# Kernel optimization log

Measured on AMD Instinct MI355X. Metric: run time of the kernel, lower is better.

The kernel has to match this reference:

```python
import jax, jax.numpy as jnp
from jax import lax
import numpy as np

B, T = 32, 15
THR1, THR2 = 15.0, 10.0  # conv1_t, conv2_t


def _conv(x, w):
    # x: (B,T,C,H,W) cumulative potentials/spikes; conv applied per timestep
    b, t, c, h, wd = x.shape
    y = lax.conv_general_dilated(x.reshape(b * t, c, h, wd), w, (1, 1), 'VALID',
                                 dimension_numbers=('NCHW', 'OIHW', 'NCHW'))
    return y.reshape(b, t, *y.shape[1:])


def _pool(x, k, s):
    b, t, c, h, wd = x.shape
    y = lax.reduce_window(x.reshape(b * t, c, h, wd), -jnp.inf, lax.max,
                          (1, 1, k, k), (1, 1, s, s), 'VALID')
    return y.reshape(b, t, *y.shape[1:])


def _pad(x, p):
    return jnp.pad(x, ((0, 0), (0, 0), (0, 0), (p, p), (p, p)))


def _fire(pot, thr):
    # sf.fire: F.threshold_(pot, thr, 0); spk = sign
    th = jnp.where(pot > thr, pot, 0.0)
    return jnp.sign(th), th


def _winner_class(pot, spk):
    # sf.get_k_winners(pot, kwta=1, r=0, spk): earliest spike, tie-break by potential
    b, t = spk.shape[:2]
    cnt = spk.sum(axis=1)                                   # (B,F,H,W) spike counts
    first = jnp.clip((t - cnt).astype(jnp.int32), 0, t - 1)  # earliest spike time
    vals = jnp.take_along_axis(pot, first[:, None], axis=1)[:, 0]  # pot at spike time
    trunc = spk * vals[:, None]                              # (B,T,F,H,W)
    v = trunc.reshape(b, -1).max(axis=1) * t                 # dominance offset per sample
    total = (trunc + spk * v[:, None, None, None, None]).sum(axis=1)  # (B,F,H,W)
    flat = total.reshape(b, -1)
    idx = jnp.argmax(flat, axis=1)
    mx = jnp.max(flat, axis=1)
    hw = pot.shape[-1] * pot.shape[-2]
    feat = idx // hw
    # decision_map: 10 classes x 20 features each -> class = feat // 20; -1 if no spike
    return jnp.where(mx != 0, feat // 20, -1).astype(jnp.int32)


def setup_inputs() -> dict:
    key = jax.random.key(0)
    k1, k2, k3, k4 = jax.random.split(key, 4)
    # cumulative binary spike wave: neuron fires at t_fire and stays 1 afterwards
    t_fire = jax.random.randint(k1, (B, 18, 32, 32), 0, T + 1)
    inp = (jnp.arange(T)[None, :, None, None, None] >= t_fire[:, None]).astype(jnp.float32)
    w1 = 0.8 + 0.05 * jax.random.normal(k2, (90, 18, 7, 7), dtype=jnp.float32)
    w2 = 0.8 + 0.05 * jax.random.normal(k3, (250, 90, 5, 5), dtype=jnp.float32)
    w3 = 0.8 + 0.05 * jax.random.normal(k4, (200, 250, 5, 5), dtype=jnp.float32)
    return {'input': inp, 'w1': w1, 'w2': w2, 'w3': w3, 'max_layer': 3}


def reference(input, w1, w2, w3, max_layer):
    # eval-mode forward of CIFAR10Net
    x = _pad(input, 2)                       # (B,T,18,36,36)
    spk1, pot1 = _fire(_conv(x, w1), THR1)   # (B,T,90,30,30)
    if max_layer == 1:
        return spk1, pot1
    spk2, pot2 = _fire(_conv(_pad(_pool(spk1, 2, 2), 1), w2), THR2)  # (B,T,250,13,13)
    if max_layer == 2:
        return spk2, pot2
    pot3 = _conv(_pad(_pool(spk2, 3, 3), 2), w3)   # (B,T,200,4,4)
    t = pot3.shape[1]
    mask = (jnp.arange(t) == t - 1).astype(pot3.dtype)[None, :, None, None, None]
    spk3 = jnp.sign(pot3 * mask)             # fire with threshold=None: only last step
    cls = _winner_class(pot3, spk3)          # (B,) predicted class or -1
    return cls, pot3
```

## Files before the change

kernel.cpp:

```cpp
#include <hip/hip_runtime.h>

#define NB 32
#define NT 15


__device__ __forceinline__ float gather8(const int* lst, int i, const char* wb) {
    int4 p0 = *(const int4*)(lst + i);
    int4 p1 = *(const int4*)(lst + i + 4);
    int o0 = __builtin_amdgcn_readfirstlane(p0.x);
    int o1 = __builtin_amdgcn_readfirstlane(p0.y);
    int o2 = __builtin_amdgcn_readfirstlane(p0.z);
    int o3 = __builtin_amdgcn_readfirstlane(p0.w);
    int o4 = __builtin_amdgcn_readfirstlane(p1.x);
    int o5 = __builtin_amdgcn_readfirstlane(p1.y);
    int o6 = __builtin_amdgcn_readfirstlane(p1.z);
    int o7 = __builtin_amdgcn_readfirstlane(p1.w);
    float a0 = *(const float*)(wb + o0);
    float a1 = *(const float*)(wb + o1);
    float a2 = *(const float*)(wb + o2);
    float a3 = *(const float*)(wb + o3);
    float a4 = *(const float*)(wb + o4);
    float a5 = *(const float*)(wb + o5);
    float a6 = *(const float*)(wb + o6);
    float a7 = *(const float*)(wb + o7);
    return ((a0 + a1) + (a2 + a3)) + ((a4 + a5) + (a6 + a7));
}

__device__ __forceinline__ void tr_tile(const float* __restrict__ src, float* __restrict__ dst,
                                        int F, int K, int KK, int CIN, int nkt, int t, int tid) {
    __shared__ float lds[32][33];
    int kt = t % nkt, ft = t / nkt;
    int k0 = kt * 32, f0 = ft * 32;
    int tx = tid & 31, ty = tid >> 5;
#pragma unroll
    for (int i = 0; i < 4; i++) {
        int fl = ty + 8 * i;
        int f = f0 + fl, k = k0 + tx;
        lds[fl][tx] = (f < F && k < K) ? src[(size_t)f * K + k] : 0.f;
    }
    __syncthreads();
#pragma unroll
    for (int i = 0; i < 4; i++) {
        int row = ty + 8 * i;
        int k = k0 + row, f = f0 + tx;
        if (k < K && f < F) {
            int j = (k % KK) * CIN + k / KK;
            dst[(size_t)j * F + f] = lds[tx][row];
        }
    }
}

__global__ __launch_bounds__(256) void k_pre(const float* __restrict__ inp,
                                             const float* __restrict__ w1,
                                             const float* __restrict__ w2,
                                             const float* __restrict__ w3,
                                             float* __restrict__ wT1, float* __restrict__ wT2,
                                             float* __restrict__ wT3,
                                             unsigned char* __restrict__ zmap,
                                             float* __restrict__ PosS2, float* __restrict__ PosS3,
                                             float* __restrict__ Pmin1,
                                             unsigned char* __restrict__ ft1,
                                             unsigned char* __restrict__ zmaps) {
    int blk = blockIdx.x, tid = threadIdx.x;
    if (blk < 2024) {
        const float* src; float* dst;
        int F, K, KK, CIN, nkt, t;
        if (blk < 84)       { src = w1; dst = wT1; F = 90;  K = 882;  KK = 49; CIN = 18;  nkt = 28;  t = blk; }
        else if (blk < 652) { src = w2; dst = wT2; F = 250; K = 2250; KK = 25; CIN = 90;  nkt = 71;  t = blk - 84; }
        else                { src = w3; dst = wT3; F = 200; K = 6250; KK = 25; CIN = 250; nkt = 196; t = blk - 652; }
        tr_tile(src, dst, F, K, KK, CIN, nkt, t, tid);
    } else if (blk == 2024) {
        if (tid < 90)  wT1[882 * 90 + tid] = 0.f;
        if (tid < 250) wT2[(size_t)2250 * 250 + tid] = 0.f;
        if (tid < 200) wT3[(size_t)6250 * 200 + tid] = 0.f;
    } else if (blk < 2187) {
        int idx = (blk - 2025) * 256 + tid;
        int xx = idx % 36, rest = idx / 36;
        int yy = rest % 36; int b = rest / 36;
        int z = 0;
        int x = xx - 2, y = yy - 2;
        if (x >= 0 && x < 32 && y >= 0 && y < 32) {
            const float* p = inp + (size_t)b * NT * 18 * 1024 + y * 32 + x;
#pragma unroll
            for (int c = 0; c < 18; c++) z += (p[(size_t)c * 1024] != 0.f);
        }
        zmap[idx] = (unsigned char)z;
    } else if (blk < 2212) {
        int idx = (blk - 2187) * 256 + tid;
        if (idx < 6250) {
            int f = idx / 25, pos = idx - f * 25;
            float acc = 0.f;
            for (int c = 0; c < 90; c++) acc += w2[(size_t)(f * 90 + c) * 25 + pos];
            PosS2[pos * 256 + f] = acc;
        }
    } else if (blk < 2232) {
        int idx = (blk - 2212) * 256 + tid;
        if (idx < 5000) {
            int f = idx / 25, pos = idx - f * 25;
            float acc = 0.f;
            for (int c = 0; c < 250; c++) acc += w3[(size_t)(f * 250 + c) * 25 + pos];
            PosS3[pos * 200 + f] = acc;
        }
    } else if (blk < 2272) {
        int bb = blk - 2232;
        __shared__ float wm[4];
        float m = 1e30f;
#pragma unroll
        for (int k = 0; k < 8; k++) {
            int i = bb * 2048 + k * 256 + tid;
            if (i < 90 * 882) m = fminf(m, w1[i]);
        }
        for (int o = 32; o > 0; o >>= 1) m = fminf(m, __shfl_down(m, o));
        if ((tid & 63) == 0) wm[tid >> 6] = m;
        __syncthreads();
        if (tid == 0) Pmin1[bb] = fminf(fminf(wm[0], wm[1]), fminf(wm[2], wm[3]));
    } else if (blk < 2905) {
        int i = (blk - 2272) * 256 + tid;
        if (i < 162000) ((uint4*)ft1)[i] = uint4{0, 0, 0, 0};
    } else {
        int i = (blk - 2905) * 256 + tid;
        if (i < 2150) ((uint4*)zmaps)[i] = uint4{0, 0, 0, 0};
    }
}

__global__ __launch_bounds__(256) void k_screen1(const unsigned char* __restrict__ zmap,
                                                 const float* __restrict__ Pmin1,
                                                 const float* __restrict__ PosS2,
                                                 const float* __restrict__ PosS3,
                                                 float* __restrict__ W2e, float* __restrict__ W3s,
                                                 int* __restrict__ cnt, int* __restrict__ list1) {
    int blk = blockIdx.x, tid = threadIdx.x;
    if (blk < 113) {
        int idx = blk * 256 + tid;
        if (idx < 28800) {
            int b = idx / 900, p = idx - b * 900;
            int oy = p / 30, ox = p - oy * 30;
            float m1 = 1e30f;
            for (int i = 0; i < 40; i++) m1 = fminf(m1, Pmin1[i]);
            int c0 = 0;
            const unsigned char* zb = zmap + (b * 36 + oy) * 36 + ox;
#pragma unroll
            for (int dy = 0; dy < 7; dy++)
#pragma unroll
                for (int dx = 0; dx < 7; dx++) c0 += zb[dy * 36 + dx];
            if (!((float)c0 * m1 > 15.0f)) {
                int pos = atomicAdd(cnt + 0, 1);
                list1[pos] = idx;
            }
        }
    } else if (blk < 282) {
        int p = blk - 113;
        int oy = p / 13, ox = p - oy * 13;
        int f = tid < 250 ? tid : 249;
        float W = 0.f;
#pragma unroll
        for (int pos = 0; pos < 25; pos++) {
            int r = pos / 5, x = pos - r * 5;
            int gy = oy + r, gx = ox + x;
            if (!(gy == 0 || gy == 16 || gx == 0 || gx == 16)) W += PosS2[pos * 256 + f];
        }
        if (tid < 250) W2e[p * 256 + tid] = W;
    } else {
        int i = (blk - 282) * 256 + tid;
        if (i < 3200) {
            int px = i / 200, f = i - px * 200;
            int oy = px >> 2, ox = px & 3;
            int r0 = max(0, 2 - oy), r1 = min(4, 5 - oy);
            int x0 = max(0, 2 - ox), x1 = min(4, 5 - ox);
            float s = 0.f;
            for (int r = r0; r <= r1; r++)
                for (int x = x0; x <= x1; x++) s += PosS3[(r * 5 + x) * 200 + f];
            W3s[px * 200 + f] = s;
        }
    }
}

__global__ __launch_bounds__(256) void k_hard1_fill(const float* __restrict__ inp,
                                                    const float* __restrict__ wT1,
                                                    const float* __restrict__ W2e,
                                                    const float* __restrict__ W3s,
                                                    const int* __restrict__ cnt,
                                                    const int* __restrict__ list1,
                                                    unsigned char* __restrict__ ft1,
                                                    unsigned char* __restrict__ nzc1,
                                                    unsigned char* __restrict__ ft2,
                                                    unsigned char* __restrict__ nz2any,
                                                    float* __restrict__ out) {
    __shared__ __align__(16) int slist[896];
    __shared__ int scnt, spcnt;
    int blk = blockIdx.x, tid = threadIdx.x;
    if (blk < 900) {
        int n = cnt[0];
        for (int it = blk; it < n; it += 900) {
            __syncthreads();
            int idx = list1[it];
            int b = idx / 900, p = idx - b * 900;
            int oy = p / 30, ox = p - oy * 30;
            unsigned char myft[4];
#pragma unroll
            for (int k = 0; k < 4; k++) {
                int j = tid + k * 256;
                unsigned char v = 255;
                if (j < 882) {
                    int dy = j / 126, rem = j - dy * 126;
                    int dx = rem / 18, c = rem - dx * 18;
                    int y = oy + dy - 2, x = ox + dx - 2;
                    v = 15;
                    if ((unsigned)y < 32u && (unsigned)x < 32u)
                        v = (inp[(size_t)b * 276480 + (size_t)c * 1024 + y * 32 + x] != 0.f) ? 0 : 200;
                }
                myft[k] = v;
            }
            int f = tid < 90 ? tid : 89;
            const char* wb = (const char*)(wT1 + f);
            const int zoff = 882 * 90 * 4;
            float acc = 0.f; int ftv = 15;
            for (int s = 0; s < 15; s++) {
                if (s == 1) {
#pragma unroll
                    for (int k = 0; k < 4; k++) {
                        if (myft[k] == 200) {
                            int j = tid + k * 256;
                            int dy = j / 126, rem = j - dy * 126;
                            int dx = rem / 18, c = rem - dx * 18;
                            int y = oy + dy - 2, x = ox + dx - 2;
                            const float* q = inp + (size_t)b * 276480 + (size_t)c * 1024 + y * 32 + x;
                            int cf = 0;
#pragma unroll
                            for (int t = 1; t < NT; t++) cf += (q[(size_t)t * 18432] != 0.f);
                            myft[k] = (unsigned char)(15 - cf);
                        }
                    }
                }
                if (tid == 0) scnt = 0;
                __syncthreads();
#pragma unroll
                for (int k = 0; k < 4; k++) {
                    if ((int)myft[k] == s) { int pp = atomicAdd(&scnt, 1); slist[pp] = (tid + k * 256) * 360; }
                }
                __syncthreads();
                if (tid == 0) {
                    int c0 = scnt, cp = (c0 + 7) & ~7;
                    for (int i = c0; i < cp; i++) slist[i] = zoff;
                    spcnt = cp;
                }
                __syncthreads();
                int e = spcnt;
                for (int i = 0; i < e; i += 8) acc += gather8(slist, i, wb);
                if (ftv == 15 && acc > 15.0f) ftv = s;
                if (__syncthreads_and(ftv != 15)) break;
            }
            if (tid < 90) {
                ft1[(size_t)idx * 90 + tid] = (unsigned char)ftv;
                if (ftv != 0) nzc1[idx] = 1;
            }
        }
    } else if (blk < 1231) {
        int i = (blk - 900) * 256 + tid;
        if (i < 84500) {
            union { unsigned char c[16]; uint4 v; } u;
            int g = i * 16;
#pragma unroll
            for (int k = 0; k < 16; k++) {
                int gg = g + k;
                int f = gg % 250;
                int p = (gg / 250) % 169;
                u.c[k] = (W2e[p * 256 + f] > 10.0f) ? 0 : 15;
            }
            *(uint4*)(ft2 + (size_t)g) = u.v;
        }
    } else if (blk == 1231) {
        if (tid < 169) {
            unsigned char any = 0;
            for (int f = 0; f < 250; f++) any |= (W2e[tid * 256 + f] <= 10.0f) ? 1 : 0;
            nz2any[tid] = any;
        }
    } else {
        int i = (blk - 1232) * 256 + tid;
        int g = i * 4;
        int px0 = g & 15;
        int f = (g >> 4) % 200;
        float4 v;
        v.x = W3s[(px0 + 0) * 200 + f];
        v.y = W3s[(px0 + 1) * 200 + f];
        v.z = W3s[(px0 + 2) * 200 + f];
        v.w = W3s[(px0 + 3) * 200 + f];
        *(float4*)(out + 32 + (size_t)g) = v;
    }
}

__global__ __launch_bounds__(256) void k_screen2(const unsigned char* __restrict__ nzc1,
                                                 const unsigned char* __restrict__ nz2any,
                                                 unsigned char* __restrict__ nzc2,
                                                 int* __restrict__ cnt, int* __restrict__ list2) {
    int idx = blockIdx.x * 256 + threadIdx.x;
    if (idx >= 5408) return;
    int b = idx / 169, p = idx - b * 169;
    int oy = p / 13, ox = p - oy * 13;
    int gy0 = max(1, oy), gy1 = min(15, oy + 4);
    int gx0 = max(1, ox), gx1 = min(15, ox + 4);
    int y0 = 2 * (gy0 - 1), y1 = 2 * (gy1 - 1) + 1;
    int x0 = 2 * (gx0 - 1), x1 = 2 * (gx1 - 1) + 1;
    int s = 0;
    const unsigned char* nb = nzc1 + b * 900;
    for (int y = y0; y <= y1; y++)
        for (int x = x0; x <= x1; x++) s += nb[y * 30 + x];
    nzc2[idx] = nz2any[p];
    if (s) { int pos = atomicAdd(cnt + 1, 1); list2[pos] = idx; }
}

__global__ __launch_bounds__(256) void k_hard2(const unsigned char* __restrict__ ft1,
                                               const float* __restrict__ wT2,
                                               const float* __restrict__ W2e,
                                               const int* __restrict__ cnt,
                                               const int* __restrict__ list2,
                                               unsigned char* __restrict__ ft2,
                                               unsigned char* __restrict__ nzc2) {
    constexpr int PADCAP = 2250 + 15 * 8;
    __shared__ __align__(16) int perm[PADCAP];
    __shared__ int start[16], cur[16];
    __shared__ int cntCs, anynz;
    int tid = threadIdx.x;
    int n = cnt[1];
    for (int it = blockIdx.x; it < n; it += 512) {
        __syncthreads();
        int idx = list2[it];
        int b = idx / 169, p = idx - b * 169;
        int oy = p / 13, ox = p - oy * 13;
        const unsigned char* fb = ft1 + (size_t)b * 81000;
        if (tid == 0) { cntCs = 0; anynz = 0; }
        if (tid < 16) cur[tid] = 0;
        unsigned char myft[9];
        int nc = 0;
#pragma unroll
        for (int k = 0; k < 9; k++) {
            int j = tid + k * 256;
            myft[k] = 0;
            if (j < 2250) {
                int r = j / 450, rem = j - r * 450;
                int x = rem / 90, c = rem - x * 90;
                int gy = oy + r, gx = ox + x;
                if (gy >= 1 && gy <= 15 && gx >= 1 && gx <= 15) {
                    const unsigned char* q = fb + ((size_t)((gy - 1) * 2) * 30 + (gx - 1) * 2) * 90 + c;
                    int m = q[0];
                    m = min(m, (int)q[90]);
                    m = min(m, (int)q[2700]);
                    m = min(m, (int)q[2790]);
                    myft[k] = (unsigned char)m;
                }
            }
            nc += (myft[k] >= 1);
        }
        for (int o = 32; o > 0; o >>= 1) nc += __shfl_down(nc, o);
        __syncthreads();
        if ((tid & 63) == 0) atomicAdd(&cntCs, nc);
        __syncthreads();
        int f = tid < 250 ? tid : 249;
        float W = W2e[p * 256 + f];
        int ftv;
        if (cntCs == 0) {
            ftv = (W > 10.0f) ? 0 : 15;
        } else {
#pragma unroll
            for (int k = 0; k < 9; k++) { int v = myft[k]; if (v >= 1) atomicAdd(&cur[v - 1], 1); }
            __syncthreads();
            if (tid == 0) {
                int s = 0;
#pragma unroll
                for (int j = 0; j < 15; j++) { int c = cur[j]; start[j] = s; s += (c + 7) & ~7; }
                start[15] = s;
            }
            __syncthreads();
            int nnzp = start[15];
            if (tid < 15) cur[tid] = start[tid];
            const int zoff = 2250 * 250 * 4;
            for (int i = tid; i < nnzp; i += 256) perm[i] = zoff;
            __syncthreads();
#pragma unroll
            for (int k = 0; k < 9; k++) {
                int v = myft[k];
                if (v >= 1) { int pp = atomicAdd(&cur[v - 1], 1); perm[pp] = (tid + k * 256) * 1000; }
            }
            __syncthreads();
            const char* wb = (const char*)(wT2 + f);
            float R = 0.f; int ft = 15;
            for (int j = 14; j >= 0; j--) {
                int sjb = start[j], e = start[j + 1];
                for (int i = sjb; i < e; i += 8) R += gather8(perm, i, wb);
                float pot = W - R;
                if (pot > 10.0f) ft = j;
                if (sjb == 0) { if (pot > 10.0f) ft = 0; break; }
                if (__all(pot <= 10.0f)) break;
            }
            ftv = ft;
        }
        if (tid < 250) {
            ft2[(size_t)idx * 250 + tid] = (unsigned char)ftv;
            if (ftv != 0) anynz = 1;
        }
        __syncthreads();
        if (tid == 0) nzc2[idx] = (unsigned char)(anynz ? 1 : 0);
    }
}

__global__ __launch_bounds__(256) void k_screen3(const unsigned char* __restrict__ nzc2,
                                                 int* __restrict__ cnt, int* __restrict__ list3) {
    int idx = blockIdx.x * 256 + threadIdx.x;
    if (idx >= 512) return;
    int b = idx >> 4, p = idx & 15;
    int oy = p >> 2, ox = p & 3;
    int r0 = max(0, 2 - oy), r1 = min(4, 5 - oy);
    int x0 = max(0, 2 - ox), x1 = min(4, 5 - ox);
    int py0 = oy + r0 - 2, py1 = oy + r1 - 2;
    int qx0 = ox + x0 - 2, qx1 = ox + x1 - 2;
    int s = 0;
    const unsigned char* nb = nzc2 + b * 169;
    for (int y = 3 * py0; y <= 3 * py1 + 2; y++)
        for (int x = 3 * qx0; x <= 3 * qx1 + 2; x++) s += nb[y * 13 + x];
    if (s) { int pos = atomicAdd(cnt + 2, 1); list3[pos] = idx; }
}

__global__ __launch_bounds__(256) void k_hard3(const unsigned char* __restrict__ ft2,
                                               const float* __restrict__ wT3,
                                               const float* __restrict__ W3s,
                                               const int* __restrict__ cnt,
                                               const int* __restrict__ list3,
                                               float* __restrict__ out) {
    constexpr int PADCAP = 4000 + 15 * 8;
    __shared__ __align__(16) int perm[PADCAP];
    __shared__ int start[16], cur[16];
    __shared__ int fbs[16], rowb[16];
    int tid = threadIdx.x;
    int n = cnt[2];
    for (int it = blockIdx.x; it < n; it += 256) {
        __syncthreads();
        int idx = list3[it];
        int b = idx >> 4, p = idx & 15;
        int oy = p >> 2, ox = p & 3;
        int r0 = max(0, 2 - oy), r1 = min(4, 5 - oy);
        int x0 = max(0, 2 - ox), x1 = min(4, 5 - ox);
        int VR = r1 - r0 + 1, VC = x1 - x0 + 1;
        int NP = VR * VC, NV = NP * 250;
        const unsigned char* fb = ft2 + (size_t)b * 42250;
        if (tid < NP) {
            int rv = tid / VC, xv = tid - rv * VC;
            int py = oy + r0 + rv - 2, pxx = ox + x0 + xv - 2;
            fbs[tid]  = (py * 3 * 13 + pxx * 3) * 250;
            rowb[tid] = ((r0 + rv) * 5 + (x0 + xv)) * 250;
        }
        if (tid < 16) cur[tid] = 0;
        __syncthreads();
        unsigned char myft[16];
#pragma unroll
        for (int k = 0; k < 16; k++) {
            int i = tid + k * 256;
            myft[k] = 0;
            if (i < NV) {
                int posv = i / 250, c = i - posv * 250;
                const unsigned char* q = fb + fbs[posv] + c;
                int m = q[0];
#pragma unroll
                for (int dy = 0; dy < 3; dy++)
#pragma unroll
                    for (int dx = 0; dx < 3; dx++)
                        if (dy | dx) m = min(m, (int)q[(dy * 13 + dx) * 250]);
                myft[k] = (unsigned char)m;
            }
        }
#pragma unroll
        for (int k = 0; k < 16; k++) { int v = myft[k]; if (v >= 1) atomicAdd(&cur[v - 1], 1); }
        __syncthreads();
        if (tid == 0) {
            int s = 0;
#pragma unroll
            for (int j = 0; j < 15; j++) { int c = cur[j]; start[j] = s; s += (c + 7) & ~7; }
            start[15] = s;
        }
        __syncthreads();
        int nnzp = start[15];
        if (tid < 15) cur[tid] = start[tid];
        const int zoff = 6250 * 200 * 4;
        for (int i = tid; i < nnzp; i += 256) perm[i] = zoff;
        __syncthreads();
#pragma unroll
        for (int k = 0; k < 16; k++) {
            int v = myft[k];
            if (v >= 1) {
                int i = tid + k * 256;
                int posv = i / 250, c = i - posv * 250;
                int pp = atomicAdd(&cur[v - 1], 1);
                perm[pp] = (rowb[posv] + c) * 800;
            }
        }
        __syncthreads();

        int f = tid < 200 ? tid : 199;
        const char* wb = (const char*)(wT3 + f);
        float W = W3s[p * 200 + f];
        float* o = out + 32 + ((size_t)b * NT) * 3200 + f * 16 + p;
        float R = 0.f;
        for (int j = 14; j >= 0; j--) {
            int sjb = start[j], e = start[j + 1];
            for (int i = sjb; i < e; i += 8) R += gather8(perm, i, wb);
            float pot = W - R;
            if (tid < 200) o[(size_t)j * 3200] = pot;
            if (sjb == 0) {
                for (int jj = j - 1; jj >= 0; jj--)
                    if (tid < 200) o[(size_t)jj * 3200] = pot;
                break;
            }
        }
    }
}

__global__ __launch_bounds__(256) void k_winner(const float* __restrict__ outp,
                                                float* __restrict__ outc) {
    int b = blockIdx.x, tid = threadIdx.x;
    const float* p14 = outp + 32 + ((size_t)b * NT + 14) * 3200;
    __shared__ float sv[256];
    __shared__ int   si[256];
    float m = 0.f;
    for (int j = tid; j < 3200; j += 256) {
        float v = p14[j];
        if (v > 0.f && v > m) m = v;
    }
    sv[tid] = m;
    __syncthreads();
    for (int s = 128; s > 0; s >>= 1) {
        if (tid < s) sv[tid] = fmaxf(sv[tid], sv[tid + s]);
        __syncthreads();
    }
    float vofs = 15.f * sv[0];
    __syncthreads();
    float bestv = 0.f; int besti = 0x3fffffff;
    for (int j = tid; j < 3200; j += 256) {
        float v = p14[j];
        float tot = (v > 0.f) ? v + vofs : 0.f;
        if (tot > bestv) { bestv = tot; besti = j; }
    }
    sv[tid] = bestv; si[tid] = besti;
    __syncthreads();
    for (int s = 128; s > 0; s >>= 1) {
        if (tid < s) {
            if (sv[tid + s] > sv[tid] || (sv[tid + s] == sv[tid] && si[tid + s] < si[tid])) {
                sv[tid] = sv[tid + s]; si[tid] = si[tid + s];
            }
        }
        __syncthreads();
    }
    if (tid == 0) {
        float mx = sv[0];
        int cls = (mx != 0.f) ? ((si[0] / 16) / 20) : -1;
        outc[b] = (float)cls;
    }
}

extern "C" void kernel_launch(void* const* d_in, const int* in_sizes, int n_in,
                              void* d_out, int out_size, void* d_ws, size_t ws_size,
                              hipStream_t stream) {
    const float* inp = (const float*)d_in[0];
    const float* w1  = (const float*)d_in[1];
    const float* w2  = (const float*)d_in[2];
    const float* w3  = (const float*)d_in[3];
    float* out = (float*)d_out;

    unsigned char* ws   = (unsigned char*)d_ws;
    unsigned char* ft1  = ws + 0;
    unsigned char* ft2  = ws + 2592000;
    float* wT1   = (float*)(ws + 3944000);
    float* wT2   = (float*)(ws + 4261888);
    float* wT3   = (float*)(ws + 6512896);
    float* PosS2 = (float*)(ws + 11513728);
    float* PosS3 = (float*)(ws + 11539328);
    float* W2e   = (float*)(ws + 11559328);
    float* W3s   = (float*)(ws + 11732384);
    float* Pmin1 = (float*)(ws + 11745184);
    unsigned char* zmap   = ws + 11745440;
    unsigned char* nzc1   = ws + 11786912;
    unsigned char* nzc2   = ws + 11815712;
    unsigned char* nz2any = ws + 11821120;
    int* cnt    = (int*)(ws + 11821296);
    int* list1  = (int*)(ws + 11821312);
    int* list2  = (int*)(ws + 11936512);
    int* list3  = (int*)(ws + 11958144);

    hipLaunchKernelGGL(k_pre, dim3(2914), dim3(256), 0, stream,
                       inp, w1, w2, w3, wT1, wT2, wT3, zmap, PosS2, PosS3, Pmin1, ft1, nzc1);
    hipLaunchKernelGGL(k_screen1, dim3(295), dim3(256), 0, stream,
                       zmap, Pmin1, PosS2, PosS3, W2e, W3s, cnt, list1);
    hipLaunchKernelGGL(k_hard1_fill, dim3(2732), dim3(256), 0, stream,
                       inp, wT1, W2e, W3s, cnt, list1, ft1, nzc1, ft2, nz2any, out);
    hipLaunchKernelGGL(k_screen2, dim3(22), dim3(256), 0, stream, nzc1, nz2any, nzc2, cnt, list2);
    hipLaunchKernelGGL(k_hard2, dim3(512), dim3(256), 0, stream, ft1, wT2, W2e, cnt, list2, ft2, nzc2);
    hipLaunchKernelGGL(k_screen3, dim3(2), dim3(256), 0, stream, nzc2, cnt, list3);
    hipLaunchKernelGGL(k_hard3, dim3(256), dim3(256), 0, stream, ft2, wT3, W3s, cnt, list3, out);
    hipLaunchKernelGGL(k_winner, dim3(NB), dim3(256), 0, stream, out, out);
}
```

Baseline: 155.8 us.

## Fuse all stages into one persistent kernel with grid-wide atomic barriers

Merges the eight separate kernel launches into a single persistent kernel of 256 blocks. Each former launch becomes a grid-stride loop over virtual blocks, and stages are separated by a global atomic-counter barrier reset by a memset. This is meant to remove per-launch overhead and the drain/fill gaps between dependent stages. In exchange, the stages with large grids (2914 and 2732 blocks) now run with only 256 resident blocks, the barriers spin-wait, and correctness depends on all blocks being co-resident.

```diff
diff --git a/kernel.cpp b/kernel.cpp
--- a/kernel.cpp
+++ b/kernel.cpp
@@ -2,7 +2,20 @@
 
 #define NB 32
 #define NT 15
-
+#define NBLK 256
+
+
+__device__ __forceinline__ void gbar(int* bar, int id) {
+    __syncthreads();
+    if (threadIdx.x == 0) {
+        __threadfence();
+        __hip_atomic_fetch_add(&bar[id], 1, __ATOMIC_ACQ_REL, __HIP_MEMORY_SCOPE_AGENT);
+        while (__hip_atomic_load(&bar[id], __ATOMIC_ACQUIRE, __HIP_MEMORY_SCOPE_AGENT) < NBLK)
+            __builtin_amdgcn_s_sleep(1);
+        __threadfence();
+    }
+    __syncthreads();
+}
 
 __device__ __forceinline__ float gather8(const int* lst, int i, const char* wb) {
     int4 p0 = *(const int4*)(lst + i);
@@ -48,150 +61,147 @@
             dst[(size_t)j * F + f] = lds[tx][row];
         }
     }
+    __syncthreads();
 }
 
-__global__ __launch_bounds__(256) void k_pre(const float* __restrict__ inp,
+__global__ __launch_bounds__(256) void k_all(const float* __restrict__ inp,
                                              const float* __restrict__ w1,
                                              const float* __restrict__ w2,
                                              const float* __restrict__ w3,
                                              float* __restrict__ wT1, float* __restrict__ wT2,
                                              float* __restrict__ wT3,
+                                             float* __restrict__ PosS2, float* __restrict__ PosS3,
+                                             float* __restrict__ W2e, float* __restrict__ W3s,
+                                             float* __restrict__ Pmin1,
                                              unsigned char* __restrict__ zmap,
-                                             float* __restrict__ PosS2, float* __restrict__ PosS3,
-                                             float* __restrict__ Pmin1,
                                              unsigned char* __restrict__ ft1,
-                                             unsigned char* __restrict__ zmaps) {
+                                             unsigned char* __restrict__ ft2,
+                                             unsigned char* __restrict__ nzc1,
+                                             unsigned char* __restrict__ nzc2,
+                                             unsigned char* __restrict__ nz2any,
+                                             int* __restrict__ cnt,
+                                             int* __restrict__ list1, int* __restrict__ list2,
+                                             int* __restrict__ list3,
+                                             int* __restrict__ bar,
+                                             float* __restrict__ out) {
     int blk = blockIdx.x, tid = threadIdx.x;
-    if (blk < 2024) {
-        const float* src; float* dst;
-        int F, K, KK, CIN, nkt, t;
-        if (blk < 84)       { src = w1; dst = wT1; F = 90;  K = 882;  KK = 49; CIN = 18;  nkt = 28;  t = blk; }
-        else if (blk < 652) { src = w2; dst = wT2; F = 250; K = 2250; KK = 25; CIN = 90;  nkt = 71;  t = blk - 84; }
-        else                { src = w3; dst = wT3; F = 200; K = 6250; KK = 25; CIN = 250; nkt = 196; t = blk - 652; }
-        tr_tile(src, dst, F, K, KK, CIN, nkt, t, tid);
-    } else if (blk == 2024) {
-        if (tid < 90)  wT1[882 * 90 + tid] = 0.f;
-        if (tid < 250) wT2[(size_t)2250 * 250 + tid] = 0.f;
-        if (tid < 200) wT3[(size_t)6250 * 200 + tid] = 0.f;
-    } else if (blk < 2187) {
-        int idx = (blk - 2025) * 256 + tid;
-        int xx = idx % 36, rest = idx / 36;
-        int yy = rest % 36; int b = rest / 36;
-        int z = 0;
-        int x = xx - 2, y = yy - 2;
-        if (x >= 0 && x < 32 && y >= 0 && y < 32) {
-            const float* p = inp + (size_t)b * NT * 18 * 1024 + y * 32 + x;
-#pragma unroll
-            for (int c = 0; c < 18; c++) z += (p[(size_t)c * 1024] != 0.f);
-        }
-        zmap[idx] = (unsigned char)z;
-    } else if (blk < 2212) {
-        int idx = (blk - 2187) * 256 + tid;
-        if (idx < 6250) {
-            int f = idx / 25, pos = idx - f * 25;
-            float acc = 0.f;
-            for (int c = 0; c < 90; c++) acc += w2[(size_t)(f * 90 + c) * 25 + pos];
-            PosS2[pos * 256 + f] = acc;
-        }
-    } else if (blk < 2232) {
-        int idx = (blk - 2212) * 256 + tid;
-        if (idx < 5000) {
-            int f = idx / 25, pos = idx - f * 25;
-            float acc = 0.f;
-            for (int c = 0; c < 250; c++) acc += w3[(size_t)(f * 250 + c) * 25 + pos];
-            PosS3[pos * 200 + f] = acc;
-        }
-    } else if (blk < 2272) {
-        int bb = blk - 2232;
-        __shared__ float wm[4];
-        float m = 1e30f;
-#pragma unroll
-        for (int k = 0; k < 8; k++) {
-            int i = bb * 2048 + k * 256 + tid;
-            if (i < 90 * 882) m = fminf(m, w1[i]);
-        }
-        for (int o = 32; o > 0; o >>= 1) m = fminf(m, __shfl_down(m, o));
-        if ((tid & 63) == 0) wm[tid >> 6] = m;
-        __syncthreads();
-        if (tid == 0) Pmin1[bb] = fminf(fminf(wm[0], wm[1]), fminf(wm[2], wm[3]));
-    } else if (blk < 2905) {
-        int i = (blk - 2272) * 256 + tid;
-        if (i < 162000) ((uint4*)ft1)[i] = uint4{0, 0, 0, 0};
-    } else {
-        int i = (blk - 2905) * 256 + tid;
-        if (i < 2150) ((uint4*)zmaps)[i] = uint4{0, 0, 0, 0};
-    }
-}
-
-__global__ __launch_bounds__(256) void k_screen1(const unsigned char* __restrict__ zmap,
-                                                 const float* __restrict__ Pmin1,
-                                                 const float* __restrict__ PosS2,
-                                                 const float* __restrict__ PosS3,
-                                                 float* __restrict__ W2e, float* __restrict__ W3s,
-                                                 int* __restrict__ cnt, int* __restrict__ list1) {
-    int blk = blockIdx.x, tid = threadIdx.x;
-    if (blk < 113) {
-        int idx = blk * 256 + tid;
-        if (idx < 28800) {
-            int b = idx / 900, p = idx - b * 900;
-            int oy = p / 30, ox = p - oy * 30;
-            float m1 = 1e30f;
-            for (int i = 0; i < 40; i++) m1 = fminf(m1, Pmin1[i]);
-            int c0 = 0;
-            const unsigned char* zb = zmap + (b * 36 + oy) * 36 + ox;
-#pragma unroll
-            for (int dy = 0; dy < 7; dy++)
-#pragma unroll
-                for (int dx = 0; dx < 7; dx++) c0 += zb[dy * 36 + dx];
-            if (!((float)c0 * m1 > 15.0f)) {
-                int pos = atomicAdd(cnt + 0, 1);
-                list1[pos] = idx;
-            }
-        }
-    } else if (blk < 282) {
-        int p = blk - 113;
-        int oy = p / 13, ox = p - oy * 13;
-        int f = tid < 250 ? tid : 249;
-        float W = 0.f;
-#pragma unroll
-        for (int pos = 0; pos < 25; pos++) {
-            int r = pos / 5, x = pos - r * 5;
-            int gy = oy + r, gx = ox + x;
-            if (!(gy == 0 || gy == 16 || gx == 0 || gx == 16)) W += PosS2[pos * 256 + f];
-        }
-        if (tid < 250) W2e[p * 256 + tid] = W;
-    } else {
-        int i = (blk - 282) * 256 + tid;
-        if (i < 3200) {
-            int px = i / 200, f = i - px * 200;
-            int oy = px >> 2, ox = px & 3;
-            int r0 = max(0, 2 - oy), r1 = min(4, 5 - oy);
-            int x0 = max(0, 2 - ox), x1 = min(4, 5 - ox);
-            float s = 0.f;
-            for (int r = r0; r <= r1; r++)
-                for (int x = x0; x <= x1; x++) s += PosS3[(r * 5 + x) * 200 + f];
-            W3s[px * 200 + f] = s;
-        }
-    }
-}
-
-__global__ __launch_bounds__(256) void k_hard1_fill(const float* __restrict__ inp,
-                                                    const float* __restrict__ wT1,
-                                                    const float* __restrict__ W2e,
-                                                    const float* __restrict__ W3s,
-                                                    const int* __restrict__ cnt,
-                                                    const int* __restrict__ list1,
-                                                    unsigned char* __restrict__ ft1,
-                                                    unsigned char* __restrict__ nzc1,
-                                                    unsigned char* __restrict__ ft2,
-                                                    unsigned char* __restrict__ nz2any,
-                                                    float* __restrict__ out) {
-    __shared__ __align__(16) int slist[896];
-    __shared__ int scnt, spcnt;
-    int blk = blockIdx.x, tid = threadIdx.x;
-    if (blk < 900) {
-        int n = cnt[0];
-        for (int it = blk; it < n; it += 900) {
+
+    for (int vb = blk; vb < 2914; vb += NBLK) {
+        if (vb < 2024) {
+            const float* src; float* dst;
+            int F, K, KK, CIN, nkt, t;
+            if (vb < 84)       { src = w1; dst = wT1; F = 90;  K = 882;  KK = 49; CIN = 18;  nkt = 28;  t = vb; }
+            else if (vb < 652) { src = w2; dst = wT2; F = 250; K = 2250; KK = 25; CIN = 90;  nkt = 71;  t = vb - 84; }
+            else               { src = w3; dst = wT3; F = 200; K = 6250; KK = 25; CIN = 250; nkt = 196; t = vb - 652; }
+            tr_tile(src, dst, F, K, KK, CIN, nkt, t, tid);
+        } else if (vb == 2024) {
+            if (tid < 90)  wT1[882 * 90 + tid] = 0.f;
+            if (tid < 250) wT2[(size_t)2250 * 250 + tid] = 0.f;
+            if (tid < 200) wT3[(size_t)6250 * 200 + tid] = 0.f;
+        } else if (vb < 2187) {
+            int idx = (vb - 2025) * 256 + tid;
+            int xx = idx % 36, rest = idx / 36;
+            int yy = rest % 36; int b = rest / 36;
+            int z = 0;
+            int x = xx - 2, y = yy - 2;
+            if (x >= 0 && x < 32 && y >= 0 && y < 32) {
+                const float* p = inp + (size_t)b * NT * 18 * 1024 + y * 32 + x;
+#pragma unroll
+                for (int c = 0; c < 18; c++) z += (p[(size_t)c * 1024] != 0.f);
+            }
+            zmap[idx] = (unsigned char)z;
+        } else if (vb < 2212) {
+            int idx = (vb - 2187) * 256 + tid;
+            if (idx < 6250) {
+                int f = idx / 25, pos = idx - f * 25;
+                float acc = 0.f;
+                for (int c = 0; c < 90; c++) acc += w2[(size_t)(f * 90 + c) * 25 + pos];
+                PosS2[pos * 256 + f] = acc;
+            }
+        } else if (vb < 2232) {
+            int idx = (vb - 2212) * 256 + tid;
+            if (idx < 5000) {
+                int f = idx / 25, pos = idx - f * 25;
+                float acc = 0.f;
+                for (int c = 0; c < 250; c++) acc += w3[(size_t)(f * 250 + c) * 25 + pos];
+                PosS3[pos * 200 + f] = acc;
+            }
+        } else if (vb < 2272) {
+            int bb = vb - 2232;
+            __shared__ float wm[4];
+            float m = 1e30f;
+#pragma unroll
+            for (int k = 0; k < 8; k++) {
+                int i = bb * 2048 + k * 256 + tid;
+                if (i < 90 * 882) m = fminf(m, w1[i]);
+            }
+            for (int o = 32; o > 0; o >>= 1) m = fminf(m, __shfl_down(m, o));
+            if ((tid & 63) == 0) wm[tid >> 6] = m;
+            __syncthreads();
+            if (tid == 0) Pmin1[bb] = fminf(fminf(wm[0], wm[1]), fminf(wm[2], wm[3]));
+            __syncthreads();
+        } else if (vb < 2905) {
+            int i = (vb - 2272) * 256 + tid;
+            if (i < 162000) ((uint4*)ft1)[i] = uint4{0, 0, 0, 0};
+        } else {
+            int i = (vb - 2905) * 256 + tid;
+            if (i < 2150) ((uint4*)nzc1)[i] = uint4{0, 0, 0, 0};
+        }
+    }
+    gbar(bar, 0);
+
+    for (int vb = blk; vb < 295; vb += NBLK) {
+        if (vb < 113) {
+            int idx = vb * 256 + tid;
+            if (idx < 28800) {
+                int b = idx / 900, p = idx - b * 900;
+                int oy = p / 30, ox = p - oy * 30;
+                float m1 = 1e30f;
+                for (int i = 0; i < 40; i++) m1 = fminf(m1, Pmin1[i]);
+                int c0 = 0;
+                const unsigned char* zb = zmap + (b * 36 + oy) * 36 + ox;
+#pragma unroll
+                for (int dy = 0; dy < 7; dy++)
+#pragma unroll
+                    for (int dx = 0; dx < 7; dx++) c0 += zb[dy * 36 + dx];
+                if (!((float)c0 * m1 > 15.0f)) {
+                    int pos = atomicAdd(cnt + 0, 1);
+                    list1[pos] = idx;
+                }
+            }
+        } else if (vb < 282) {
+            int p = vb - 113;
+            int oy = p / 13, ox = p - oy * 13;
+            int f = tid < 250 ? tid : 249;
+            float W = 0.f;
+#pragma unroll
+            for (int pos = 0; pos < 25; pos++) {
+                int r = pos / 5, x = pos - r * 5;
+                int gy = oy + r, gx = ox + x;
+                if (!(gy == 0 || gy == 16 || gx == 0 || gx == 16)) W += PosS2[pos * 256 + f];
+            }
+            if (tid < 250) W2e[p * 256 + tid] = W;
+        } else {
+            int i = (vb - 282) * 256 + tid;
+            if (i < 3200) {
+                int px = i / 200, f = i - px * 200;
+                int oy = px >> 2, ox = px & 3;
+                int r0 = max(0, 2 - oy), r1 = min(4, 5 - oy);
+                int x0 = max(0, 2 - ox), x1 = min(4, 5 - ox);
+                float s = 0.f;
+                for (int r = r0; r <= r1; r++)
+                    for (int x = x0; x <= x1; x++) s += PosS3[(r * 5 + x) * 200 + f];
+                W3s[px * 200 + f] = s;
+            }
+        }
+    }
+    gbar(bar, 1);
+
+    {
+        __shared__ __align__(16) int slist[896];
+        __shared__ int scnt, spcnt;
+        int n1 = __hip_atomic_load(&cnt[0], __ATOMIC_RELAXED, __HIP_MEMORY_SCOPE_AGENT);
+        for (int it = blk; it < n1; it += NBLK) {
             __syncthreads();
             int idx = list1[it];
             int b = idx / 900, p = idx - b * 900;
@@ -254,115 +264,214 @@
                 ft1[(size_t)idx * 90 + tid] = (unsigned char)ftv;
                 if (ftv != 0) nzc1[idx] = 1;
             }
-        }
-    } else if (blk < 1231) {
-        int i = (blk - 900) * 256 + tid;
-        if (i < 84500) {
-            union { unsigned char c[16]; uint4 v; } u;
-            int g = i * 16;
+            __syncthreads();
+        }
+        for (int vb = blk; vb < 1832; vb += NBLK) {
+            if (vb < 331) {
+                int i = vb * 256 + tid;
+                if (i < 84500) {
+                    union { unsigned char c[16]; uint4 v; } u;
+                    int g = i * 16;
+#pragma unroll
+                    for (int k = 0; k < 16; k++) {
+                        int gg = g + k;
+                        int f = gg % 250;
+                        int p = (gg / 250) % 169;
+                        u.c[k] = (W2e[p * 256 + f] > 10.0f) ? 0 : 15;
+                    }
+                    *(uint4*)(ft2 + (size_t)g) = u.v;
+                }
+            } else if (vb == 331) {
+                if (tid < 169) {
+                    unsigned char any = 0;
+                    for (int f = 0; f < 250; f++) any |= (W2e[tid * 256 + f] <= 10.0f) ? 1 : 0;
+                    nz2any[tid] = any;
+                }
+            } else {
+                int i = (vb - 332) * 256 + tid;
+                int g = i * 4;
+                int px0 = g & 15;
+                int f = (g >> 4) % 200;
+                float4 v;
+                v.x = W3s[(px0 + 0) * 200 + f];
+                v.y = W3s[(px0 + 1) * 200 + f];
+                v.z = W3s[(px0 + 2) * 200 + f];
+                v.w = W3s[(px0 + 3) * 200 + f];
+                *(float4*)(out + 32 + (size_t)g) = v;
+            }
+        }
+    }
+    gbar(bar, 2);
+
+    {
+        int idx = blk * 256 + tid;
+        if (idx < 5408) {
+            int b = idx / 169, p = idx - b * 169;
+            int oy = p / 13, ox = p - oy * 13;
+            int gy0 = max(1, oy), gy1 = min(15, oy + 4);
+            int gx0 = max(1, ox), gx1 = min(15, ox + 4);
+            int y0 = 2 * (gy0 - 1), y1 = 2 * (gy1 - 1) + 1;
+            int x0 = 2 * (gx0 - 1), x1 = 2 * (gx1 - 1) + 1;
+            int s = 0;
+            const unsigned char* nb = nzc1 + b * 900;
+            for (int y = y0; y <= y1; y++)
+                for (int x = x0; x <= x1; x++) s += nb[y * 30 + x];
+            nzc2[idx] = nz2any[p];
+            if (s) { int pos = atomicAdd(cnt + 1, 1); list2[pos] = idx; }
+        }
+    }
+    gbar(bar, 3);
+
+    {
+        constexpr int PADCAP = 2250 + 15 * 8;
+        __shared__ __align__(16) int perm[PADCAP];
+        __shared__ int start[16], cur[16];
+        __shared__ int cntCs, anynz;
+        int n2 = __hip_atomic_load(&cnt[1], __ATOMIC_RELAXED, __HIP_MEMORY_SCOPE_AGENT);
+        for (int it = blk; it < n2; it += NBLK) {
+            __syncthreads();
+            int idx = list2[it];
+            int b = idx / 169, p = idx - b * 169;
+            int oy = p / 13, ox = p - oy * 13;
+            const unsigned char* fb = ft1 + (size_t)b * 81000;
+            if (tid == 0) { cntCs = 0; anynz = 0; }
+            if (tid < 16) cur[tid] = 0;
+            unsigned char myft[9];
+            int nc = 0;
+#pragma unroll
+            for (int k = 0; k < 9; k++) {
+                int j = tid + k * 256;
+                myft[k] = 0;
+                if (j < 2250) {
+                    int r = j / 450, rem = j - r * 450;
+                    int x = rem / 90, c = rem - x * 90;
+                    int gy = oy + r, gx = ox + x;
+                    if (gy >= 1 && gy <= 15 && gx >= 1 && gx <= 15) {
+                        const unsigned char* q = fb + ((size_t)((gy - 1) * 2) * 30 + (gx - 1) * 2) * 90 + c;
+                        int m = q[0];
+                        m = min(m, (int)q[90]);
+                        m = min(m, (int)q[2700]);
+                        m = min(m, (int)q[2790]);
+                        myft[k] = (unsigned char)m;
+                    }
+                }
+                nc += (myft[k] >= 1);
+            }
+            for (int o = 32; o > 0; o >>= 1) nc += __shfl_down(nc, o);
+            __syncthreads();
+            if ((tid & 63) == 0) atomicAdd(&cntCs, nc);
+            __syncthreads();
+            int f = tid < 250 ? tid : 249;
+            float W = W2e[p * 256 + f];
+            int ftv;
+            if (cntCs == 0) {
+                ftv = (W > 10.0f) ? 0 : 15;
+            } else {
+#pragma unroll
+                for (int k = 0; k < 9; k++) { int v = myft[k]; if (v >= 1) atomicAdd(&cur[v - 1], 1); }
+                __syncthreads();
+                if (tid == 0) {
+                    int s = 0;
+#pragma unroll
+                    for (int j = 0; j < 15; j++) { int c = cur[j]; start[j] = s; s += (c + 7) & ~7; }
+                    start[15] = s;
+                }
+                __syncthreads();
+                int nnzp = start[15];
+                if (tid < 15) cur[tid] = start[tid];
+                const int zoff = 2250 * 250 * 4;
+                for (int i = tid; i < nnzp; i += 256) perm[i] = zoff;
+                __syncthreads();
+#pragma unroll
+                for (int k = 0; k < 9; k++) {
+                    int v = myft[k];
+                    if (v >= 1) { int pp = atomicAdd(&cur[v - 1], 1); perm[pp] = (tid + k * 256) * 1000; }
+                }
+                __syncthreads();
+                const char* wb = (const char*)(wT2 + f);
+                float R = 0.f; int ft = 15;
+                for (int j = 14; j >= 0; j--) {
+                    int sjb = start[j], e = start[j + 1];
+                    for (int i = sjb; i < e; i += 8) R += gather8(perm, i, wb);
+                    float pot = W - R;
+                    if (pot > 10.0f) ft = j;
+                    if (sjb == 0) { if (pot > 10.0f) ft = 0; break; }
+                    if (__all(pot <= 10.0f)) break;
+                }
+                ftv = ft;
+            }
+            if (tid < 250) {
+                ft2[(size_t)idx * 250 + tid] = (unsigned char)ftv;
+                if (ftv != 0) anynz = 1;
+            }
+            __syncthreads();
+            if (tid == 0) nzc2[idx] = (unsigned char)(anynz ? 1 : 0);
+            __syncthreads();
+        }
+    }
+    gbar(bar, 4);
+
+    {
+        int idx = blk * 256 + tid;
+        if (idx < 512) {
+            int b = idx >> 4, p = idx & 15;
+            int oy = p >> 2, ox = p & 3;
+            int r0 = max(0, 2 - oy), r1 = min(4, 5 - oy);
+            int x0 = max(0, 2 - ox), x1 = min(4, 5 - ox);
+            int py0 = oy + r0 - 2, py1 = oy + r1 - 2;
+            int qx0 = ox + x0 - 2, qx1 = ox + x1 - 2;
+            int s = 0;
+            const unsigned char* nb = nzc2 + b * 169;
+            for (int y = 3 * py0; y <= 3 * py1 + 2; y++)
+                for (int x = 3 * qx0; x <= 3 * qx1 + 2; x++) s += nb[y * 13 + x];
+            if (s) { int pos = atomicAdd(cnt + 2, 1); list3[pos] = idx; }
+        }
+    }
+    gbar(bar, 5);
+
+    {
+        constexpr int PADCAP = 4000 + 15 * 8;
+        __shared__ __align__(16) int perm[PADCAP];
+        __shared__ int start[16], cur[16];
+        __shared__ int fbs[16], rowb[16];
+        int n3 = __hip_atomic_load(&cnt[2], __ATOMIC_RELAXED, __HIP_MEMORY_SCOPE_AGENT);
+        for (int it = blk; it < n3; it += NBLK) {
+            __syncthreads();
+            int idx = list3[it];
+            int b = idx >> 4, p = idx & 15;
+            int oy = p >> 2, ox = p & 3;
+            int r0 = max(0, 2 - oy), r1 = min(4, 5 - oy);
+            int x0 = max(0, 2 - ox), x1 = min(4, 5 - ox);
+            int VR = r1 - r0 + 1, VC = x1 - x0 + 1;
+            int NP = VR * VC, NV = NP * 250;
+            const unsigned char* fb = ft2 + (size_t)b * 42250;
+            if (tid < NP) {
+                int rv = tid / VC, xv = tid - rv * VC;
+                int py = oy + r0 + rv - 2, pxx = ox + x0 + xv - 2;
+                fbs[tid]  = (py * 3 * 13 + pxx * 3) * 250;
+                rowb[tid] = ((r0 + rv) * 5 + (x0 + xv)) * 250;
+            }
+            if (tid < 16) cur[tid] = 0;
+            __syncthreads();
+            unsigned char myft[16];
 #pragma unroll
             for (int k = 0; k < 16; k++) {
-                int gg = g + k;
-                int f = gg % 250;
-                int p = (gg / 250) % 169;
-                u.c[k] = (W2e[p * 256 + f] > 10.0f) ? 0 : 15;
-            }
-            *(uint4*)(ft2 + (size_t)g) = u.v;
-        }
-    } else if (blk == 1231) {
-        if (tid < 169) {
-            unsigned char any = 0;
-            for (int f = 0; f < 250; f++) any |= (W2e[tid * 256 + f] <= 10.0f) ? 1 : 0;
-            nz2any[tid] = any;
-        }
-    } else {
-        int i = (blk - 1232) * 256 + tid;
-        int g = i * 4;
-        int px0 = g & 15;
-        int f = (g >> 4) % 200;
-        float4 v;
-        v.x = W3s[(px0 + 0) * 200 + f];
-        v.y = W3s[(px0 + 1) * 200 + f];
-        v.z = W3s[(px0 + 2) * 200 + f];
-        v.w = W3s[(px0 + 3) * 200 + f];
-        *(float4*)(out + 32 + (size_t)g) = v;
-    }
-}
-
-__global__ __launch_bounds__(256) void k_screen2(const unsigned char* __restrict__ nzc1,
-                                                 const unsigned char* __restrict__ nz2any,
-                                                 unsigned char* __restrict__ nzc2,
-                                                 int* __restrict__ cnt, int* __restrict__ list2) {
-    int idx = blockIdx.x * 256 + threadIdx.x;
-    if (idx >= 5408) return;
-    int b = idx / 169, p = idx - b * 169;
-    int oy = p / 13, ox = p - oy * 13;
-    int gy0 = max(1, oy), gy1 = min(15, oy + 4);
-    int gx0 = max(1, ox), gx1 = min(15, ox + 4);
-    int y0 = 2 * (gy0 - 1), y1 = 2 * (gy1 - 1) + 1;
-    int x0 = 2 * (gx0 - 1), x1 = 2 * (gx1 - 1) + 1;
-    int s = 0;
-    const unsigned char* nb = nzc1 + b * 900;
-    for (int y = y0; y <= y1; y++)
-        for (int x = x0; x <= x1; x++) s += nb[y * 30 + x];
-    nzc2[idx] = nz2any[p];
-    if (s) { int pos = atomicAdd(cnt + 1, 1); list2[pos] = idx; }
-}
-
-__global__ __launch_bounds__(256) void k_hard2(const unsigned char* __restrict__ ft1,
-                                               const float* __restrict__ wT2,
-                                               const float* __restrict__ W2e,
-                                               const int* __restrict__ cnt,
-                                               const int* __restrict__ list2,
-                                               unsigned char* __restrict__ ft2,
-                                               unsigned char* __restrict__ nzc2) {
-    constexpr int PADCAP = 2250 + 15 * 8;
-    __shared__ __align__(16) int perm[PADCAP];
-    __shared__ int start[16], cur[16];
-    __shared__ int cntCs, anynz;
-    int tid = threadIdx.x;
-    int n = cnt[1];
-    for (int it = blockIdx.x; it < n; it += 512) {
-        __syncthreads();
-        int idx = list2[it];
-        int b = idx / 169, p = idx - b * 169;
-        int oy = p / 13, ox = p - oy * 13;
-        const unsigned char* fb = ft1 + (size_t)b * 81000;
-        if (tid == 0) { cntCs = 0; anynz = 0; }
-        if (tid < 16) cur[tid] = 0;
-        unsigned char myft[9];
-        int nc = 0;
-#pragma unroll
-        for (int k = 0; k < 9; k++) {
-            int j = tid + k * 256;
-            myft[k] = 0;
-            if (j < 2250) {
-                int r = j / 450, rem = j - r * 450;
-                int x = rem / 90, c = rem - x * 90;
-                int gy = oy + r, gx = ox + x;
-                if (gy >= 1 && gy <= 15 && gx >= 1 && gx <= 15) {
-                    const unsigned char* q = fb + ((size_t)((gy - 1) * 2) * 30 + (gx - 1) * 2) * 90 + c;
+                int i = tid + k * 256;
+                myft[k] = 0;
+                if (i < NV) {
+                    int posv = i / 250, c = i - posv * 250;
+                    const unsigned char* q = fb + fbs[posv] + c;
                     int m = q[0];
-                    m = min(m, (int)q[90]);
-                    m = min(m, (int)q[2700]);
-                    m = min(m, (int)q[2790]);
+#pragma unroll
+                    for (int dy = 0; dy < 3; dy++)
+#pragma unroll
+                        for (int dx = 0; dx < 3; dx++)
+                            if (dy | dx) m = min(m, (int)q[(dy * 13 + dx) * 250]);
                     myft[k] = (unsigned char)m;
                 }
             }
-            nc += (myft[k] >= 1);
-        }
-        for (int o = 32; o > 0; o >>= 1) nc += __shfl_down(nc, o);
-        __syncthreads();
-        if ((tid & 63) == 0) atomicAdd(&cntCs, nc);
-        __syncthreads();
-        int f = tid < 250 ? tid : 249;
-        float W = W2e[p * 256 + f];
-        int ftv;
-        if (cntCs == 0) {
-            ftv = (W > 10.0f) ? 0 : 15;
-        } else {
-#pragma unroll
-            for (int k = 0; k < 9; k++) { int v = myft[k]; if (v >= 1) atomicAdd(&cur[v - 1], 1); }
+#pragma unroll
+            for (int k = 0; k < 16; k++) { int v = myft[k]; if (v >= 1) atomicAdd(&cur[v - 1], 1); }
             __syncthreads();
             if (tid == 0) {
                 int s = 0;
@@ -373,185 +482,81 @@
             __syncthreads();
             int nnzp = start[15];
             if (tid < 15) cur[tid] = start[tid];
-            const int zoff = 2250 * 250 * 4;
+            const int zoff = 6250 * 200 * 4;
             for (int i = tid; i < nnzp; i += 256) perm[i] = zoff;
             __syncthreads();
 #pragma unroll
-            for (int k = 0; k < 9; k++) {
+            for (int k = 0; k < 16; k++) {
                 int v = myft[k];
-                if (v >= 1) { int pp = atomicAdd(&cur[v - 1], 1); perm[pp] = (tid + k * 256) * 1000; }
-            }
-            __syncthreads();
-            const char* wb = (const char*)(wT2 + f);
-            float R = 0.f; int ft = 15;
+                if (v >= 1) {
+                    int i = tid + k * 256;
+                    int posv = i / 250, c = i - posv * 250;
+                    int pp = atomicAdd(&cur[v - 1], 1);
+                    perm[pp] = (rowb[posv] + c) * 800;
+                }
+            }
+            __syncthreads();
+
+            int f = tid < 200 ? tid : 199;
+            const char* wb = (const char*)(wT3 + f);
+            float W = W3s[p * 200 + f];
+            float* o = out + 32 + ((size_t)b * NT) * 3200 + f * 16 + p;
+            float R = 0.f;
             for (int j = 14; j >= 0; j--) {
                 int sjb = start[j], e = start[j + 1];
                 for (int i = sjb; i < e; i += 8) R += gather8(perm, i, wb);
                 float pot = W - R;
-                if (pot > 10.0f) ft = j;
-                if (sjb == 0) { if (pot > 10.0f) ft = 0; break; }
-                if (__all(pot <= 10.0f)) break;
-            }
-            ftv = ft;
-        }
-        if (tid < 250) {
-            ft2[(size_t)idx * 250 + tid] = (unsigned char)ftv;
-            if (ftv != 0) anynz = 1;
-        }
+                if (tid < 200) o[(size_t)j * 3200] = pot;
+                if (sjb == 0) {
+                    for (int jj = j - 1; jj >= 0; jj--)
+                        if (tid < 200) o[(size_t)jj * 3200] = pot;
+                    break;
+                }
+            }
+            __syncthreads();
+        }
+    }
+    gbar(bar, 6);
+
+    if (blk < NB) {
+        int b = blk;
+        const float* p14 = out + 32 + ((size_t)b * NT + 14) * 3200;
+        __shared__ float sv[256];
+        __shared__ int   si[256];
+        float m = 0.f;
+        for (int j = tid; j < 3200; j += 256) {
+            float v = p14[j];
+            if (v > 0.f && v > m) m = v;
+        }
+        sv[tid] = m;
         __syncthreads();
-        if (tid == 0) nzc2[idx] = (unsigned char)(anynz ? 1 : 0);
-    }
-}
-
-__global__ __launch_bounds__(256) void k_screen3(const unsigned char* __restrict__ nzc2,
-                                                 int* __restrict__ cnt, int* __restrict__ list3) {
-    int idx = blockIdx.x * 256 + threadIdx.x;
-    if (idx >= 512) return;
-    int b = idx >> 4, p = idx & 15;
-    int oy = p >> 2, ox = p & 3;
-    int r0 = max(0, 2 - oy), r1 = min(4, 5 - oy);
-    int x0 = max(0, 2 - ox), x1 = min(4, 5 - ox);
-    int py0 = oy + r0 - 2, py1 = oy + r1 - 2;
-    int qx0 = ox + x0 - 2, qx1 = ox + x1 - 2;
-    int s = 0;
-    const unsigned char* nb = nzc2 + b * 169;
-    for (int y = 3 * py0; y <= 3 * py1 + 2; y++)
-        for (int x = 3 * qx0; x <= 3 * qx1 + 2; x++) s += nb[y * 13 + x];
-    if (s) { int pos = atomicAdd(cnt + 2, 1); list3[pos] = idx; }
-}
-
-__global__ __launch_bounds__(256) void k_hard3(const unsigned char* __restrict__ ft2,
-                                               const float* __restrict__ wT3,
-                                               const float* __restrict__ W3s,
-                                               const int* __restrict__ cnt,
-                                               const int* __restrict__ list3,
-                                               float* __restrict__ out) {
-    constexpr int PADCAP = 4000 + 15 * 8;
-    __shared__ __align__(16) int perm[PADCAP];
-    __shared__ int start[16], cur[16];
-    __shared__ int fbs[16], rowb[16];
-    int tid = threadIdx.x;
-    int n = cnt[2];
-    for (int it = blockIdx.x; it < n; it += 256) {
+        for (int s = 128; s > 0; s >>= 1) {
+            if (tid < s) sv[tid] = fmaxf(sv[tid], sv[tid + s]);
+            __syncthreads();
+        }
+        float vofs = 15.f * sv[0];
         __syncthreads();
-        int idx = list3[it];
-        int b = idx >> 4, p = idx & 15;
-        int oy = p >> 2, ox = p & 3;
-        int r0 = max(0, 2 - oy), r1 = min(4, 5 - oy);
-        int x0 = max(0, 2 - ox), x1 = min(4, 5 - ox);
-        int VR = r1 - r0 + 1, VC = x1 - x0 + 1;
-        int NP = VR * VC, NV = NP * 250;
-        const unsigned char* fb = ft2 + (size_t)b * 42250;
-        if (tid < NP) {
-            int rv = tid / VC, xv = tid - rv * VC;
-            int py = oy + r0 + rv - 2, pxx = ox + x0 + xv - 2;
-            fbs[tid]  = (py * 3 * 13 + pxx * 3) * 250;
-            rowb[tid] = ((r0 + rv) * 5 + (x0 + xv)) * 250;
-        }
-        if (tid < 16) cur[tid] = 0;
+        float bestv = 0.f; int besti = 0x3fffffff;
+        for (int j = tid; j < 3200; j += 256) {
+            float v = p14[j];
+            float tot = (v > 0.f) ? v + vofs : 0.f;
+            if (tot > bestv) { bestv = tot; besti = j; }
+        }
+        sv[tid] = bestv; si[tid] = besti;
         __syncthreads();
-        unsigned char myft[16];
-#pragma unroll
-        for (int k = 0; k < 16; k++) {
-            int i = tid + k * 256;
-            myft[k] = 0;
-            if (i < NV) {
-                int posv = i / 250, c = i - posv * 250;
-                const unsigned char* q = fb + fbs[posv] + c;
-                int m = q[0];
-#pragma unroll
-                for (int dy = 0; dy < 3; dy++)
-#pragma unroll
-                    for (int dx = 0; dx < 3; dx++)
-                        if (dy | dx) m = min(m, (int)q[(dy * 13 + dx) * 250]);
-                myft[k] = (unsigned char)m;
-            }
-        }
-#pragma unroll
-        for (int k = 0; k < 16; k++) { int v = myft[k]; if (v >= 1) atomicAdd(&cur[v - 1], 1); }
-        __syncthreads();
+        for (int s = 128; s > 0; s >>= 1) {
+            if (tid < s) {
+                if (sv[tid + s] > sv[tid] || (sv[tid + s] == sv[tid] && si[tid + s] < si[tid])) {
+                    sv[tid] = sv[tid + s]; si[tid] = si[tid + s];
+                }
+            }
+            __syncthreads();
+        }
         if (tid == 0) {
-            int s = 0;
-#pragma unroll
-            for (int j = 0; j < 15; j++) { int c = cur[j]; start[j] = s; s += (c + 7) & ~7; }
-            start[15] = s;
-        }
-        __syncthreads();
-        int nnzp = start[15];
-        if (tid < 15) cur[tid] = start[tid];
-        const int zoff = 6250 * 200 * 4;
-        for (int i = tid; i < nnzp; i += 256) perm[i] = zoff;
-        __syncthreads();
-#pragma unroll
-        for (int k = 0; k < 16; k++) {
-            int v = myft[k];
-            if (v >= 1) {
-                int i = tid + k * 256;
-                int posv = i / 250, c = i - posv * 250;
-                int pp = atomicAdd(&cur[v - 1], 1);
-                perm[pp] = (rowb[posv] + c) * 800;
-            }
-        }
-        __syncthreads();
-
-        int f = tid < 200 ? tid : 199;
-        const char* wb = (const char*)(wT3 + f);
-        float W = W3s[p * 200 + f];
-        float* o = out + 32 + ((size_t)b * NT) * 3200 + f * 16 + p;
-        float R = 0.f;
-        for (int j = 14; j >= 0; j--) {
-            int sjb = start[j], e = start[j + 1];
-            for (int i = sjb; i < e; i += 8) R += gather8(perm, i, wb);
-            float pot = W - R;
-            if (tid < 200) o[(size_t)j * 3200] = pot;
-            if (sjb == 0) {
-                for (int jj = j - 1; jj >= 0; jj--)
-                    if (tid < 200) o[(size_t)jj * 3200] = pot;
-                break;
-            }
-        }
-    }
-}
-
-__global__ __launch_bounds__(256) void k_winner(const float* __restrict__ outp,
-                                                float* __restrict__ outc) {
-    int b = blockIdx.x, tid = threadIdx.x;
-    const float* p14 = outp + 32 + ((size_t)b * NT + 14) * 3200;
-    __shared__ float sv[256];
-    __shared__ int   si[256];
-    float m = 0.f;
-    for (int j = tid; j < 3200; j += 256) {
-        float v = p14[j];
-        if (v > 0.f && v > m) m = v;
-    }
-    sv[tid] = m;
-    __syncthreads();
-    for (int s = 128; s > 0; s >>= 1) {
-        if (tid < s) sv[tid] = fmaxf(sv[tid], sv[tid + s]);
-        __syncthreads();
-    }
-    float vofs = 15.f * sv[0];
-    __syncthreads();
-    float bestv = 0.f; int besti = 0x3fffffff;
-    for (int j = tid; j < 3200; j += 256) {
-        float v = p14[j];
-        float tot = (v > 0.f) ? v + vofs : 0.f;
-        if (tot > bestv) { bestv = tot; besti = j; }
-    }
-    sv[tid] = bestv; si[tid] = besti;
-    __syncthreads();
-    for (int s = 128; s > 0; s >>= 1) {
-        if (tid < s) {
-            if (sv[tid + s] > sv[tid] || (sv[tid + s] == sv[tid] && si[tid + s] < si[tid])) {
-                sv[tid] = sv[tid + s]; si[tid] = si[tid + s];
-            }
-        }
-        __syncthreads();
-    }
-    if (tid == 0) {
-        float mx = sv[0];
-        int cls = (mx != 0.f) ? ((si[0] / 16) / 20) : -1;
-        outc[b] = (float)cls;
+            float mx = sv[0];
+            int cls = (mx != 0.f) ? ((si[0] / 16) / 20) : -1;
+            out[b] = (float)cls;
+        }
     }
 }
 
@@ -583,16 +588,10 @@
     int* list1  = (int*)(ws + 11821312);
     int* list2  = (int*)(ws + 11936512);
     int* list3  = (int*)(ws + 11958144);
-
-    hipLaunchKernelGGL(k_pre, dim3(2914), dim3(256), 0, stream,
-                       inp, w1, w2, w3, wT1, wT2, wT3, zmap, PosS2, PosS3, Pmin1, ft1, nzc1);
-    hipLaunchKernelGGL(k_screen1, dim3(295), dim3(256), 0, stream,
-                       zmap, Pmin1, PosS2, PosS3, W2e, W3s, cnt, list1);
-    hipLaunchKernelGGL(k_hard1_fill, dim3(2732), dim3(256), 0, stream,
-                       inp, wT1, W2e, W3s, cnt, list1, ft1, nzc1, ft2, nz2any, out);
-    hipLaunchKernelGGL(k_screen2, dim3(22), dim3(256), 0, stream, nzc1, nz2any, nzc2, cnt, list2);
-    hipLaunchKernelGGL(k_hard2, dim3(512), dim3(256), 0, stream, ft1, wT2, W2e, cnt, list2, ft2, nzc2);
-    hipLaunchKernelGGL(k_screen3, dim3(2), dim3(256), 0, stream, nzc2, cnt, list3);
-    hipLaunchKernelGGL(k_hard3, dim3(256), dim3(256), 0, stream, ft2, wT3, W3s, cnt, list3, out);
-    hipLaunchKernelGGL(k_winner, dim3(NB), dim3(256), 0, stream, out, out);
+    int* bar    = (int*)(ws + 11960192);
+
+    hipMemsetAsync(bar, 0, 32, stream);
+    hipLaunchKernelGGL(k_all, dim3(NBLK), dim3(256), 0, stream,
+                       inp, w1, w2, w3, wT1, wT2, wT3, PosS2, PosS3, W2e, W3s, Pmin1,
+                       zmap, ft1, ft2, nzc1, nzc2, nz2any, cnt, list1, list2, list3, bar, out);
 }
```

After: 414.8 us. 2.66x slower.
